# Kernel tuning notes

Measured on AMD Instinct MI355X. Metric: run time of the kernel, lower is better.

## Reference

```python
import jax, jax.numpy as jnp
import numpy as np

SIGMA = 1.0
B, M, D = 32, 4, 196608  # groups, matrix_size, flattened feature dim (3*256*256)


def _mmd_kernel_mean(x, y, w):
    # x, y: [B, m, D] float32; w: [B]
    # Faithful to kernel_fn: dist = sqrt(clamp(sum((x-y)^2), 1e-12)) / D / sigma
    # Pairwise squared distances via gram expansion (avoids materializing [B,m,m,D]).
    xn = jnp.sum(x * x, axis=-1)                     # [B, m]
    yn = jnp.sum(y * y, axis=-1)                     # [B, m]
    xy = jnp.einsum('bid,bjd->bij', x, y)            # [B, m, m]
    d2 = jnp.maximum(xn[:, :, None] + yn[:, None, :] - 2.0 * xy, 1e-12)
    denom = float(D) if D > 0 else 1.0
    sigma = max(float(SIGMA), 1e-6)
    dist = jnp.sqrt(d2) / denom / sigma              # [B, m, m]
    expo = jnp.clip(-dist * w[:, None, None], -1e6, 0.0)
    k = jnp.nan_to_num(jnp.exp(expo), nan=0.0, posinf=0.0, neginf=0.0)
    return jnp.nan_to_num(jnp.mean(k, axis=(1, 2)), nan=0.0)  # [B]


def setup_inputs() -> dict:
    key = jax.random.key(0)
    k1, k2, k3, k4 = jax.random.split(key, 4)
    return {
        'f_st': jax.random.normal(k1, (B, M, D), dtype=jnp.float32),
        'f_sr': jax.random.normal(k2, (B, M, D), dtype=jnp.float32),
        'wt': jax.random.uniform(k3, (B,), dtype=jnp.float32),
        'wtout': jax.random.uniform(k4, (B,), dtype=jnp.float32),
    }


def reference(f_st, f_sr, wt, wtout):
    f_st = f_st.astype(jnp.float32)
    f_sr = f_sr.astype(jnp.float32)
    inter_sample = _mmd_kernel_mean(f_st, f_st, wt)
    inter_gt = _mmd_kernel_mean(f_sr, f_sr, wt)
    cross = _mmd_kernel_mean(f_st, f_sr, wt)
    loss_raw = jnp.nan_to_num(inter_sample + inter_gt - 2.0 * cross, nan=0.0)
    loss = jnp.nan_to_num(wtout * loss_raw, nan=0.0)
    return jnp.mean(loss)
```

## Files before the change

kernel.cpp:

```cpp
#include <hip/hip_runtime.h>


constexpr int NB = 32;
constexpr int MM = 4;
constexpr int DD = 196608;
constexpr int D4 = DD / 4;
constexpr int BPG = 16;
constexpr int NTHREADS = 256;
constexpr int CHUNK4 = D4 / BPG;
constexpr int TB = 256;
constexpr int NITER = CHUNK4 / TB;
constexpr int NACC = 36;

__device__ __forceinline__ void gl_lds16(const float4* gsrc, float4* lds_dst) {
    __builtin_amdgcn_global_load_lds(
        (const __attribute__((address_space(1))) void*)gsrc,
        (__attribute__((address_space(3))) void*)lds_dst,
        16, 0, 0);
}

__device__ __forceinline__ float dot4(const float4& a, const float4& b) {
    return a.x * b.x + a.y * b.y + a.z * b.z + a.w * b.w;
}

__global__ __launch_bounds__(NTHREADS) void mmd_partial_kernel(
    const float* __restrict__ st, const float* __restrict__ sr,
    float* __restrict__ partial)
{
    __shared__ float4 buf[2][8][TB];

    const int b   = blockIdx.x / BPG;
    const int blk = blockIdx.x % BPG;
    const int c0  = blk * CHUNK4;

    const float4* stb = reinterpret_cast<const float4*>(st) + (size_t)b * MM * D4;
    const float4* srb = reinterpret_cast<const float4*>(sr) + (size_t)b * MM * D4;

    const float4* rowp[8];
#pragma unroll
    for (int r = 0; r < 4; ++r) rowp[r]     = stb + (size_t)r * D4 + c0;
#pragma unroll
    for (int r = 0; r < 4; ++r) rowp[4 + r] = srb + (size_t)r * D4 + c0;

    const int wave = threadIdx.x >> 6;
    const int lane = threadIdx.x & 63;

    auto stage = [&](int cur, int it) {
        const int cc = it * TB;
#pragma unroll
        for (int rr = 0; rr < 2; ++rr) {
            const int r = 2 * wave + rr;
            const float4* src = rowp[r] + cc + lane;
#pragma unroll
            for (int q = 0; q < 4; ++q) {
                gl_lds16(src + q * 64, &buf[cur][r][q * 64]);
            }
        }
    };

    float acc[NACC];
#pragma unroll
    for (int k = 0; k < NACC; ++k) acc[k] = 0.0f;

    stage(0, 0);

    for (int it = 0; it < NITER; ++it) {
        const int cur = it & 1;
        asm volatile("s_waitcnt vmcnt(0)");
        __syncthreads();
        if (it + 1 < NITER) stage(cur ^ 1, it + 1);

        const int col = threadIdx.x;
        float4 x[8];
#pragma unroll
        for (int r = 0; r < 8; ++r) x[r] = buf[cur][r][col];

        int k = 0;
#pragma unroll
        for (int i = 0; i < MM; ++i)
#pragma unroll
            for (int j = i; j < MM; ++j) { acc[k] += dot4(x[i], x[j]); ++k; }
#pragma unroll
        for (int i = 0; i < MM; ++i)
#pragma unroll
            for (int j = i; j < MM; ++j) { acc[k] += dot4(x[4 + i], x[4 + j]); ++k; }
#pragma unroll
        for (int i = 0; i < MM; ++i)
#pragma unroll
            for (int j = 0; j < MM; ++j) { acc[k] += dot4(x[i], x[4 + j]); ++k; }
    }

#pragma unroll
    for (int k = 0; k < NACC; ++k) {
        float v = acc[k];
        for (int off = 32; off > 0; off >>= 1) v += __shfl_down(v, off, 64);
        acc[k] = v;
    }

    __shared__ float red[NTHREADS / 64][NACC];
    if (lane == 0) {
#pragma unroll
        for (int k = 0; k < NACC; ++k) red[wave][k] = acc[k];
    }
    __syncthreads();
    if (threadIdx.x < NACC) {
        const int k = threadIdx.x;
        float s = red[0][k] + red[1][k] + red[2][k] + red[3][k];
        partial[(size_t)blockIdx.x * NACC + k] = s;
    }
}

__global__ __launch_bounds__(1024) void mmd_final_kernel(
    const float* __restrict__ partial, const float* __restrict__ wt,
    const float* __restrict__ wtout, float* __restrict__ out)
{
    __shared__ float acc_s[NB][NACC];
    for (int p = threadIdx.x; p < NB * NACC; p += 1024) {
        const int b = p / NACC;
        const int k = p % NACC;
        float s = 0.0f;
        for (int blk = 0; blk < BPG; ++blk)
            s += partial[((size_t)b * BPG + blk) * NACC + k];
        acc_s[b][k] = s;
    }
    __syncthreads();

    __shared__ float lds[NB];
    const int b = threadIdx.x;
    if (b < NB) {
        const float* a = acc_s[b];
        float ss[MM][MM], rr[MM][MM], sg[MM][MM];
        {
            int k = 0;
            for (int i = 0; i < MM; ++i)
                for (int j = i; j < MM; ++j) { ss[i][j] = a[k]; ss[j][i] = a[k]; ++k; }
            for (int i = 0; i < MM; ++i)
                for (int j = i; j < MM; ++j) { rr[i][j] = a[k]; rr[j][i] = a[k]; ++k; }
            for (int i = 0; i < MM; ++i)
                for (int j = 0; j < MM; ++j) { sg[i][j] = a[k]; ++k; }
        }

        const float w    = wt[b];
        const float invD = 1.0f / (float)DD;
        auto kv = [&](float d2) -> float {
            d2 = fmaxf(d2, 1e-12f);
            float dist = sqrtf(d2) * invD;
            float e = -dist * w;
            e = fminf(fmaxf(e, -1e6f), 0.0f);
            return expf(e);
        };

        float mss = 0.0f, mrr = 0.0f, msr = 0.0f;
        for (int i = 0; i < MM; ++i) {
            for (int j = 0; j < MM; ++j) {
                mss += kv(ss[i][i] + ss[j][j] - 2.0f * ss[i][j]);
                mrr += kv(rr[i][i] + rr[j][j] - 2.0f * rr[i][j]);
                msr += kv(ss[i][i] + rr[j][j] - 2.0f * sg[i][j]);
            }
        }
        const float inv16 = 1.0f / 16.0f;
        float loss_raw = mss * inv16 + mrr * inv16 - 2.0f * (msr * inv16);
        lds[b] = wtout[b] * loss_raw;
    }
    __syncthreads();
    if (threadIdx.x == 0) {
        float s = 0.0f;
        for (int i = 0; i < NB; ++i) s += lds[i];
        out[0] = s / (float)NB;
    }
}

extern "C" void kernel_launch(void* const* d_in, const int* in_sizes, int n_in,
                              void* d_out, int out_size, void* d_ws, size_t ws_size,
                              hipStream_t stream) {
    const float* f_st  = (const float*)d_in[0];
    const float* f_sr  = (const float*)d_in[1];
    const float* wt    = (const float*)d_in[2];
    const float* wtout = (const float*)d_in[3];
    float* out     = (float*)d_out;
    float* partial = (float*)d_ws;

    mmd_partial_kernel<<<NB * BPG, NTHREADS, 0, stream>>>(f_st, f_sr, partial);
    mmd_final_kernel<<<1, 1024, 0, stream>>>(partial, wt, wtout, out);
}
```

Baseline: 44.42 us.

## Use single-wave blocks with barrier-free triple-buffered LDS prefetch

Each block is now a single 64-thread wave, and each batch is split across 48 blocks instead of 16. The LDS staging is triple-buffered with a prefetch distance of two and partial vmcnt waits, so __syncthreads disappears and more loads stay in flight. The loop is fully unrolled, and each wave writes its partial sums directly instead of doing a cross-wave LDS reduction. The partial workspace becomes three times larger, and the final kernel sums more partials per batch.

```diff
diff --git a/kernel.cpp b/kernel.cpp
--- a/kernel.cpp
+++ b/kernel.cpp
@@ -5,11 +5,12 @@
 constexpr int MM = 4;
 constexpr int DD = 196608;
 constexpr int D4 = DD / 4;
-constexpr int BPG = 16;
-constexpr int NTHREADS = 256;
+constexpr int BPG = 48;
+constexpr int NTHREADS = 64;
 constexpr int CHUNK4 = D4 / BPG;
-constexpr int TB = 256;
+constexpr int TB = 64;
 constexpr int NITER = CHUNK4 / TB;
+constexpr int NBUF = 3;
 constexpr int NACC = 36;
 
 __device__ __forceinline__ void gl_lds16(const float4* gsrc, float4* lds_dst) {
@@ -19,75 +20,76 @@
         16, 0, 0);
 }
 
-__device__ __forceinline__ float dot4(const float4& a, const float4& b) {
-    return a.x * b.x + a.y * b.y + a.z * b.z + a.w * b.w;
-}
-
 __global__ __launch_bounds__(NTHREADS) void mmd_partial_kernel(
     const float* __restrict__ st, const float* __restrict__ sr,
     float* __restrict__ partial)
 {
-    __shared__ float4 buf[2][8][TB];
+    __shared__ float4 buf[NBUF][8][TB];
 
-    const int b   = blockIdx.x / BPG;
-    const int blk = blockIdx.x % BPG;
-    const int c0  = blk * CHUNK4;
+    const int b    = blockIdx.x / BPG;
+    const int blk  = blockIdx.x % BPG;
+    const int c0   = blk * CHUNK4;
+    const int lane = threadIdx.x;
 
     const float4* stb = reinterpret_cast<const float4*>(st) + (size_t)b * MM * D4;
     const float4* srb = reinterpret_cast<const float4*>(sr) + (size_t)b * MM * D4;
 
-    const float4* rowp[8];
+    const float4* srcp[8];
 #pragma unroll
-    for (int r = 0; r < 4; ++r) rowp[r]     = stb + (size_t)r * D4 + c0;
+    for (int r = 0; r < 4; ++r) srcp[r]     = stb + (size_t)r * D4 + c0 + lane;
 #pragma unroll
-    for (int r = 0; r < 4; ++r) rowp[4 + r] = srb + (size_t)r * D4 + c0;
+    for (int r = 0; r < 4; ++r) srcp[4 + r] = srb + (size_t)r * D4 + c0 + lane;
 
-    const int wave = threadIdx.x >> 6;
-    const int lane = threadIdx.x & 63;
-
-    auto stage = [&](int cur, int it) {
-        const int cc = it * TB;
+    auto stage = [&](int s) {
+        const int cur = s % NBUF;
 #pragma unroll
-        for (int rr = 0; rr < 2; ++rr) {
-            const int r = 2 * wave + rr;
-            const float4* src = rowp[r] + cc + lane;
-#pragma unroll
-            for (int q = 0; q < 4; ++q) {
-                gl_lds16(src + q * 64, &buf[cur][r][q * 64]);
-            }
-        }
+        for (int r = 0; r < 8; ++r)
+            gl_lds16(srcp[r] + s * TB, &buf[cur][r][0]);
     };
 
     float acc[NACC];
 #pragma unroll
     for (int k = 0; k < NACC; ++k) acc[k] = 0.0f;
 
-    stage(0, 0);
+    stage(0);
+    stage(1);
 
+#pragma unroll
     for (int it = 0; it < NITER; ++it) {
-        const int cur = it & 1;
-        asm volatile("s_waitcnt vmcnt(0)");
-        __syncthreads();
-        if (it + 1 < NITER) stage(cur ^ 1, it + 1);
+        if (it == NITER - 1) asm volatile("s_waitcnt vmcnt(0)" ::: "memory");
+        else                 asm volatile("s_waitcnt vmcnt(8)" ::: "memory");
+        if (it + 2 < NITER) stage(it + 2);
 
-        const int col = threadIdx.x;
+        const int cur = it % NBUF;
         float4 x[8];
 #pragma unroll
-        for (int r = 0; r < 8; ++r) x[r] = buf[cur][r][col];
+        for (int r = 0; r < 8; ++r) x[r] = buf[cur][r][lane];
 
         int k = 0;
 #pragma unroll
         for (int i = 0; i < MM; ++i)
 #pragma unroll
-            for (int j = i; j < MM; ++j) { acc[k] += dot4(x[i], x[j]); ++k; }
+            for (int j = i; j < MM; ++j) {
+                acc[k] += x[i].x * x[j].x + x[i].y * x[j].y +
+                          x[i].z * x[j].z + x[i].w * x[j].w;
+                ++k;
+            }
 #pragma unroll
         for (int i = 0; i < MM; ++i)
 #pragma unroll
-            for (int j = i; j < MM; ++j) { acc[k] += dot4(x[4 + i], x[4 + j]); ++k; }
+            for (int j = i; j < MM; ++j) {
+                acc[k] += x[4+i].x * x[4+j].x + x[4+i].y * x[4+j].y +
+                          x[4+i].z * x[4+j].z + x[4+i].w * x[4+j].w;
+                ++k;
+            }
 #pragma unroll
         for (int i = 0; i < MM; ++i)
 #pragma unroll
-            for (int j = 0; j < MM; ++j) { acc[k] += dot4(x[i], x[4 + j]); ++k; }
+            for (int j = 0; j < MM; ++j) {
+                acc[k] += x[i].x * x[4+j].x + x[i].y * x[4+j].y +
+                          x[i].z * x[4+j].z + x[i].w * x[4+j].w;
+                ++k;
+            }
     }
 
 #pragma unroll
@@ -96,17 +98,10 @@
         for (int off = 32; off > 0; off >>= 1) v += __shfl_down(v, off, 64);
         acc[k] = v;
     }
-
-    __shared__ float red[NTHREADS / 64][NACC];
     if (lane == 0) {
+        float* p = partial + (size_t)blockIdx.x * NACC;
 #pragma unroll
-        for (int k = 0; k < NACC; ++k) red[wave][k] = acc[k];
-    }
-    __syncthreads();
-    if (threadIdx.x < NACC) {
-        const int k = threadIdx.x;
-        float s = red[0][k] + red[1][k] + red[2][k] + red[3][k];
-        partial[(size_t)blockIdx.x * NACC + k] = s;
+        for (int k = 0; k < NACC; ++k) p[k] = acc[k];
     }
 }
 
```

Result: slower. 68.12 us (+53.4%).
